# Kernel tuning notes

Measured on AMD Instinct MI355X. Metric: run time of the kernel, lower is better.

Reference implementation:

```python
import jax, jax.numpy as jnp
import numpy as np

N = 1048576
NUM_FREQS = 4
NUM_DIM = 3
NUM_QUANTS = 80
NUM_FEATS = 4
MIN_LOG2_FREQ = 1.0
MAX_LOG2_FREQ = 6.0
NUM_LINES = 2 * NUM_FREQS * NUM_DIM  # sin/cos x freq x axis = 24
LATENT = NUM_LINES * NUM_FEATS       # 96


def setup_inputs() -> dict:
    key = jax.random.key(0)
    ks = jax.random.split(key, 8)
    positions = jax.random.uniform(ks[0], (N, NUM_DIM), jnp.float32, -1.0, 1.0)
    d = jax.random.normal(ks[1], (N, NUM_DIM), jnp.float32)
    directions = d / jnp.linalg.norm(d, axis=-1, keepdims=True)
    grid = jax.random.normal(ks[2], (NUM_LINES, NUM_QUANTS, NUM_FEATS), jnp.float32) * 0.1
    w_geom1 = jax.random.normal(ks[3], (LATENT, 64), jnp.float32) * (1.0 / np.sqrt(LATENT))
    w_geom2 = jax.random.normal(ks[4], (64, 16), jnp.float32) * (1.0 / 8.0)
    w_color1 = jax.random.normal(ks[5], (31, 64), jnp.float32) * (1.0 / np.sqrt(31.0))
    w_color2 = jax.random.normal(ks[6], (64, 64), jnp.float32) * (1.0 / 8.0)
    w_color3 = jax.random.normal(ks[7], (64, 3), jnp.float32) * (1.0 / 8.0)
    return {"positions": positions, "directions": directions, "grid": grid,
            "w_geom1": w_geom1, "w_geom2": w_geom2,
            "w_color1": w_color1, "w_color2": w_color2, "w_color3": w_color3}


@jax.custom_vjp
def trunc_exp(x):
    return jnp.exp(x)

def _te_fwd(x):
    return jnp.exp(x), x

def _te_bwd(x, g):
    return (g * jnp.exp(jnp.clip(x, -15.0, 15.0)),)

trunc_exp.defvjp(_te_fwd, _te_bwd)


def spherical_harmonics16(d):
    # degree-4 (l=0..3) real SH basis, 16 components, torch-ngp coefficients
    x, y, z = d[:, 0], d[:, 1], d[:, 2]
    xx, yy, zz = x * x, y * y, z * z
    xy, yz, xz = x * y, y * z, x * z
    return jnp.stack([
        jnp.full_like(x, 0.28209479177387814),
        -0.48860251190291987 * y,
        0.48860251190291987 * z,
        -0.48860251190291987 * x,
        1.0925484305920792 * xy,
        -1.0925484305920792 * yz,
        0.94617469575755997 * zz - 0.31539156525251999,
        -1.0925484305920792 * xz,
        0.54627421529603959 * (xx - yy),
        -0.59004358992664352 * y * (3.0 * xx - yy),
        2.8906114426405538 * xy * z,
        -0.45704579946446572 * y * (4.0 * zz - xx - yy),
        0.37317633259011546 * z * (2.0 * zz - 3.0 * xx - 3.0 * yy),
        -0.45704579946446572 * x * (4.0 * zz - xx - yy),
        1.4453057213202769 * z * (xx - yy),
        -0.59004358992664352 * x * (xx - 3.0 * yy),
    ], axis=-1)  # [N, 16]


def qff1_encode(positions, grid):
    # frequencies 2^linspace(min,max,F)
    freqs = 2.0 ** jnp.linspace(MIN_LOG2_FREQ, MAX_LOG2_FREQ, NUM_FREQS).astype(jnp.float32)
    # phase: [N, D, F]
    p = positions[:, :, None] * freqs[None, None, :]
    coords = jnp.concatenate([jnp.sin(p), jnp.cos(p)], axis=-1)  # [N, D, 2F]
    coords = coords.transpose(0, 2, 1).reshape(positions.shape[0], NUM_LINES)  # [N, L]
    # map [-1,1] -> continuous grid coord and linearly interpolate 1D lines
    u = (coords + 1.0) * 0.5 * (NUM_QUANTS - 1)
    i0 = jnp.clip(jnp.floor(u).astype(jnp.int32), 0, NUM_QUANTS - 2)
    w = (u - i0.astype(u.dtype))[..., None]  # [N, L, 1]
    lidx = jnp.arange(NUM_LINES)[None, :]
    g0 = grid[lidx, i0]      # [N, L, C]
    g1 = grid[lidx, i0 + 1]  # [N, L, C]
    feat = g0 * (1.0 - w) + g1 * w
    return feat.reshape(positions.shape[0], LATENT)


def _forward(positions, directions, grid, w_geom1, w_geom2, w_color1, w_color2, w_color3):
    enc = qff1_encode(positions, grid)                    # [N, 96]
    h = jax.nn.relu(enc @ w_geom1)                        # [N, 64]
    f = h @ w_geom2                                       # [N, 16]
    raw_sigma, feature = f[:, :1], f[:, 1:]
    density = trunc_exp(raw_sigma - 1.0)                  # [N, 1]
    sh = spherical_harmonics16(directions)                # [N, 16]
    hc = jnp.concatenate([sh, feature], axis=-1)          # [N, 31]
    hc = jax.nn.relu(hc @ w_color1)
    hc = jax.nn.relu(hc @ w_color2)
    rgb = jax.nn.sigmoid(hc @ w_color3)                   # [N, 3]
    return rgb, density


def reference(positions, directions, grid, w_geom1, w_geom2, w_color1, w_color2, w_color3):
    return _forward(positions, directions, grid, w_geom1, w_geom2, w_color1, w_color2, w_color3)
```

## Files before the change

### kernel.cpp

```cpp
#include <hip/hip_runtime.h>
#include <stdint.h>


typedef _Float16 half8  __attribute__((ext_vector_type(8)));
typedef _Float16 h2     __attribute__((ext_vector_type(2)));
typedef float    f32x16 __attribute__((ext_vector_type(16)));

union FragU { uint32_t u[4]; uint4 q; half8 h; };
union H2U   { uint32_t u; h2 h; };

static __device__ __forceinline__ h2 bch2(uint32_t v) { H2U x; x.u = v; return x.h; }
static __device__ __forceinline__ uint32_t bcu(h2 v)  { H2U x; x.h = v; return x.u; }

static __device__ __forceinline__ h2 cvtpk(float lo, float hi) {
  return __builtin_bit_cast(h2, __builtin_amdgcn_cvt_pkrtz(lo, hi));
}
static __device__ __forceinline__ uint32_t pkrtz(float lo, float hi) {
  return bcu(cvtpk(lo, hi));
}
static __device__ __forceinline__ void plswap_u(uint32_t &a, uint32_t &b) {
  asm("v_permlane32_swap_b32 %0, %1" : "+v"(a), "+v"(b));
}
static __device__ __forceinline__ void plswap_f(float &a, float &b) {
  asm("v_permlane32_swap_b32 %0, %1" : "+v"(a), "+v"(b));
}
static __device__ __forceinline__ half8 mk_frag(uint32_t a, uint32_t b, uint32_t c, uint32_t d) {
  FragU f; f.u[0] = a; f.u[1] = b; f.u[2] = c; f.u[3] = d; return f.h;
}
static __device__ __forceinline__ uint32_t maxz(uint32_t v) {
  h2 h = bch2(v); h = __builtin_elementwise_max(h, (h2)(_Float16)0.0f); return bcu(h);
}
static __device__ __forceinline__ unsigned short f16b(float v) {
  _Float16 h = (_Float16)v; return __builtin_bit_cast(unsigned short, h);
}

#define MFMA(A, B, C) __builtin_amdgcn_mfma_f32_32x32x16_f16((A), (B), (C), 0, 0, 0)

#define W1OFF   0
#define W2OFF   13312
#define WC1OFF  17920
#define WC2OFF  23040
#define WC3OFF  32256
#define GROFF   36864
#define LDSZ    52224
#define WBYTES  36864

static __device__ __forceinline__ half8 ldwp(const unsigned char* s, int row, int off) {
  FragU f; f.q = *(const uint4*)(s + row + off);
  asm volatile("" : "+v"(f.u[0]), "+v"(f.u[1]), "+v"(f.u[2]), "+v"(f.u[3]));
  return f.h;
}

template<int BASE, bool RELU>
static __device__ __forceinline__ half8 packB(const f32x16& a) {
  uint32_t x = pkrtz(a[BASE + 0], a[BASE + 1]);
  uint32_t z = pkrtz(a[BASE + 2], a[BASE + 3]);
  uint32_t y = pkrtz(a[BASE + 4], a[BASE + 5]);
  uint32_t w = pkrtz(a[BASE + 6], a[BASE + 7]);
  if (RELU) { x = maxz(x); z = maxz(z); y = maxz(y); w = maxz(w); }
  plswap_u(x, y);
  plswap_u(z, w);
  return mk_frag(x, z, y, w);
}

template<int J>
static __device__ __forceinline__ void gather(const float* m, int gbase,
                                              float q0, float q1, float q2,
                                              const unsigned char* lds,
                                              uint32_t& w01, uint32_t& w23) {
  constexpr int jm = J % 6;
  constexpr int DIMP[6] = {0, 1, 1, 2, 2, 0};
  constexpr int LNS0[6] = {0, 1, 4, 5, 8, 9};
  constexpr int GOFFJ = (LNS0[jm] + (J < 6 ? 0 : 12)) * 640;
  float q = (DIMP[jm] == 0) ? q0 : ((DIMP[jm] == 1) ? q1 : q2);
  float r = fmaf(q, m[jm], (J < 6) ? 0.0f : 0.25f);
  r = __builtin_amdgcn_fractf(r);
  float s = __builtin_amdgcn_sinf(r);
  float u = fmaf(s, 39.5f, 39.5f);
  int i0 = (int)u;
  i0 = i0 < 0 ? 0 : (i0 > 78 ? 78 : i0);
  float w = u - (float)i0;
  const unsigned char* base = lds + gbase + GOFFJ + (i0 << 2);
  uint32_t a0 = *(const uint32_t*)(base);
  uint32_t b0 = *(const uint32_t*)(base + 4);
  uint32_t a1 = *(const uint32_t*)(base + 320);
  uint32_t b1 = *(const uint32_t*)(base + 324);
  h2 wh = cvtpk(w, w);
  h2 f01 = __builtin_elementwise_fma(bch2(b0) - bch2(a0), wh, bch2(a0));
  h2 f23 = __builtin_elementwise_fma(bch2(b1) - bch2(a1), wh, bch2(a1));
  w01 = bcu(f01);
  w23 = bcu(f23);
}

template<int T>
static __device__ __forceinline__ half8 enc2(const float* m, int gbase,
                                             float q0, float q1, float q2,
                                             const unsigned char* lds) {
  uint32_t a, b, c, d;
  gather<2 * T + 0>(m, gbase, q0, q1, q2, lds, a, b);
  gather<2 * T + 1>(m, gbase, q0, q1, q2, lds, c, d);
  return mk_frag(a, b, c, d);
}

__global__ __launch_bounds__(512, 2)
void qff_fwd(const float* __restrict__ pos, const float* __restrict__ dir,
             const float* __restrict__ grid,
             const float* __restrict__ w1, const float* __restrict__ w2,
             const float* __restrict__ wc1, const float* __restrict__ wc2,
             const float* __restrict__ wc3,
             float* __restrict__ out, int Npts) {
  __shared__ __align__(16) unsigned char smem[LDSZ];
  const int tid = threadIdx.x;

  for (int i = tid; i < WBYTES / 4; i += 512) ((uint32_t*)smem)[i] = 0;
  __syncthreads();
  for (int i = tid; i < 6144; i += 512)
    *(unsigned short*)(smem + W1OFF  + (i & 63) * 208 + (i >> 6) * 2) = f16b(w1[i]);
  for (int i = tid; i < 1024; i += 512)
    *(unsigned short*)(smem + W2OFF  + (i & 15) * 144 + (i >> 4) * 2) = f16b(w2[i]);
  for (int i = tid; i < 1984; i += 512)
    *(unsigned short*)(smem + WC1OFF + (i & 63) * 80  + (i >> 6) * 2) = f16b(wc1[i]);
  for (int i = tid; i < 4096; i += 512)
    *(unsigned short*)(smem + WC2OFF + (i & 63) * 144 + (i >> 6) * 2) = f16b(wc2[i]);
  for (int i = tid; i < 192; i += 512)
    *(unsigned short*)(smem + WC3OFF + (i % 3) * 144 + (i / 3) * 2) = f16b(wc3[i]);
  for (int i = tid; i < 1920; i += 512) {
    float4 v = ((const float4*)grid)[i];
    int line = i / 80, q = i - line * 80;
    uint32_t* dst = (uint32_t*)(smem + GROFF + line * 640 + q * 4);
    dst[0]  = (((uint32_t)f16b(v.y)) << 16) | f16b(v.x);
    dst[80] = (((uint32_t)f16b(v.w)) << 16) | f16b(v.z);
  }
  __syncthreads();

  const int lane = tid & 63;
  const int wid  = tid >> 6;
  const int g    = lane >> 5;
  const int o    = lane & 31;

  const int a13 = o * 208 + g * 16;
  const int a9  = o * 144 + g * 16;
  const int a5  = o * 80  + g * 16;
  half8 w1f[2][6], w2f[4], c1f[2][2], c2f[2][4], c3f[4];
#pragma unroll
  for (int t = 0; t < 6; ++t) {
    w1f[0][t] = ldwp(smem, a13, W1OFF + t * 32);
    w1f[1][t] = ldwp(smem, a13, W1OFF + 6656 + t * 32);
  }
#pragma unroll
  for (int t = 0; t < 4; ++t) {
    w2f[t]    = ldwp(smem, a9, W2OFF + t * 32);
    c2f[0][t] = ldwp(smem, a9, WC2OFF + t * 32);
    c2f[1][t] = ldwp(smem, a9, WC2OFF + 4608 + t * 32);
    c3f[t]    = ldwp(smem, a9, WC3OFF + t * 32);
  }
#pragma unroll
  for (int t = 0; t < 2; ++t) {
    c1f[0][t] = ldwp(smem, a5, WC1OFF + t * 32);
    c1f[1][t] = ldwp(smem, a5, WC1OFF + 2560 + t * 32);
  }

  constexpr float IV = 0.15915494309189535f;
  constexpr float F0 = 2.0f, F1 = 6.349604207872798f, F2 = 20.158736798317971f, F3 = 64.0f;
  const float M0c[6] = {F0*IV, F0*IV, F1*IV, F1*IV, F2*IV, F3*IV};
  const float M1c[6] = {F0*IV, F1*IV, F2*IV, F2*IV, F3*IV, F3*IV};
  float m[6];
#pragma unroll
  for (int j = 0; j < 6; ++j) m[j] = g ? M1c[j] : M0c[j];
  const int gbase = GROFF + g * 1280;

  const f32x16 Z = {0,0,0,0, 0,0,0,0, 0,0,0,0, 0,0,0,0};
  const int ntile = Npts >> 8;
  int tb = blockIdx.x;
  if (tb >= ntile) return;

  int p = (tb << 8) + (wid << 5) + o;
  float px = pos[3*p+0], py = pos[3*p+1], pz = pos[3*p+2];
  float dx = dir[3*p+0], dy = dir[3*p+1], dz = dir[3*p+2];

  for (; tb < ntile; tb += gridDim.x) {
    int tbn = tb + gridDim.x;
    int pn  = ((tbn < ntile ? tbn : ntile - 1) << 8) + (wid << 5) + o;
    float npx = pos[3*pn+0], npy = pos[3*pn+1], npz = pos[3*pn+2];
    float ndx = dir[3*pn+0], ndy = dir[3*pn+1], ndz = dir[3*pn+2];

    float q0 = g ? pz : px;
    float q1 = g ? px : py;
    float q2 = g ? py : pz;

    f32x16 acc0 = Z, acc1 = Z;
#define L1STEP(T) { half8 bf = enc2<T>(m, gbase, q0, q1, q2, smem); \
                    acc0 = MFMA(w1f[0][T], bf, acc0); \
                    acc1 = MFMA(w1f[1][T], bf, acc1); }
    L1STEP(0) L1STEP(1) L1STEP(2) L1STEP(3) L1STEP(4) L1STEP(5)
#undef L1STEP

    half8 hb0 = packB<0, true>(acc0), hb1 = packB<8, true>(acc0);
    half8 hb2 = packB<0, true>(acc1), hb3 = packB<8, true>(acc1);

    f32x16 acc2 = Z;
    acc2 = MFMA(w2f[0], hb0, acc2);
    acc2 = MFMA(w2f[1], hb1, acc2);
    acc2 = MFMA(w2f[2], hb2, acc2);
    acc2 = MFMA(w2f[3], hb3, acc2);
    float sigma = __expf(acc2[0] - 1.0f);

    float xx = dx*dx, yy = dy*dy, zz = dz*dz;
    float xy = dx*dy, yz = dy*dz, xz = dx*dz;
    float s0, s1, s2, s3, s4, s5, s6, s7;
    if (g == 0) {
      s0 = 0.28209479177387814f;
      s1 = -0.48860251190291987f * dy;
      s2 =  0.48860251190291987f * dz;
      s3 = -0.48860251190291987f * dx;
      s4 =  1.0925484305920792f * xy;
      s5 = -1.0925484305920792f * yz;
      s6 =  0.94617469575756f * zz - 0.31539156525252f;
      s7 = -1.0925484305920792f * xz;
    } else {
      s0 =  0.5462742152960396f * (xx - yy);
      s1 = -0.5900435899266435f * dy * (3.0f * xx - yy);
      s2 =  2.890611442640554f * xy * dz;
      s3 = -0.4570457994644657f * dy * (4.0f * zz - xx - yy);
      s4 =  0.37317633259011546f * dz * (2.0f * zz - 3.0f * xx - 3.0f * yy);
      s5 = -0.4570457994644657f * dx * (4.0f * zz - xx - yy);
      s6 =  1.445305721320277f * dz * (xx - yy);
      s7 = -0.5900435899266435f * dx * (xx - 3.0f * yy);
    }
    half8 shB = mk_frag(pkrtz(s0, s1), pkrtz(s2, s3), pkrtz(s4, s5), pkrtz(s6, s7));

    uint32_t e0 = pkrtz(acc2[1], acc2[2]);
    uint32_t e2 = pkrtz(acc2[5], acc2[6]);
    plswap_u(e0, e2);
    float a3 = acc2[3], b7 = acc2[7];
    plswap_f(a3, b7);
    float cc0 = acc2[0], d4 = acc2[4];
    plswap_f(cc0, d4);
    uint32_t e1 = pkrtz(a3, d4);
    uint32_t e3 = pkrtz(b7, acc2[4]);
    half8 featB = mk_frag(e0, e1, e2, e3);

    f32x16 acc3a = Z, acc3b = Z;
    acc3a = MFMA(c1f[0][0], shB,   acc3a);
    acc3a = MFMA(c1f[0][1], featB, acc3a);
    acc3b = MFMA(c1f[1][0], shB,   acc3b);
    acc3b = MFMA(c1f[1][1], featB, acc3b);

    half8 g2b0 = packB<0, true>(acc3a), g2b1 = packB<8, true>(acc3a);
    half8 g2b2 = packB<0, true>(acc3b), g2b3 = packB<8, true>(acc3b);

    f32x16 acc4a = Z, acc4b = Z;
    acc4a = MFMA(c2f[0][0], g2b0, acc4a);
    acc4a = MFMA(c2f[0][1], g2b1, acc4a);
    acc4a = MFMA(c2f[0][2], g2b2, acc4a);
    acc4a = MFMA(c2f[0][3], g2b3, acc4a);
    acc4b = MFMA(c2f[1][0], g2b0, acc4b);
    acc4b = MFMA(c2f[1][1], g2b1, acc4b);
    acc4b = MFMA(c2f[1][2], g2b2, acc4b);
    acc4b = MFMA(c2f[1][3], g2b3, acc4b);

    half8 g3b0 = packB<0, true>(acc4a), g3b1 = packB<8, true>(acc4a);
    half8 g3b2 = packB<0, true>(acc4b), g3b3 = packB<8, true>(acc4b);

    f32x16 acc5 = Z;
    acc5 = MFMA(c3f[0], g3b0, acc5);
    acc5 = MFMA(c3f[1], g3b1, acc5);
    acc5 = MFMA(c3f[2], g3b2, acc5);
    acc5 = MFMA(c3f[3], g3b3, acc5);

    if (lane < 32) {
      float rr = __builtin_amdgcn_rcpf(1.0f + __expf(-acc5[0]));
      float gg = __builtin_amdgcn_rcpf(1.0f + __expf(-acc5[1]));
      float bb = __builtin_amdgcn_rcpf(1.0f + __expf(-acc5[2]));
      out[3 * p + 0] = rr;
      out[3 * p + 1] = gg;
      out[3 * p + 2] = bb;
      out[3 * Npts + p] = sigma;
    }

    p = pn;
    px = npx; py = npy; pz = npz;
    dx = ndx; dy = ndy; dz = ndz;
  }
}

extern "C" void kernel_launch(void* const* d_in, const int* in_sizes, int n_in,
                              void* d_out, int out_size, void* d_ws, size_t ws_size,
                              hipStream_t stream) {
  const float* pos  = (const float*)d_in[0];
  const float* dirs = (const float*)d_in[1];
  const float* grid = (const float*)d_in[2];
  const float* w1   = (const float*)d_in[3];
  const float* w2   = (const float*)d_in[4];
  const float* wc1  = (const float*)d_in[5];
  const float* wc2  = (const float*)d_in[6];
  const float* wc3  = (const float*)d_in[7];
  float* out = (float*)d_out;
  const int Npts = in_sizes[0] / 3;

  qff_fwd<<<dim3(512), dim3(512), 0, stream>>>(pos, dirs, grid, w1, w2, wc1, wc2, wc3,
                                               out, Npts);
}
```

Baseline: 53.44 us.

## Reload MLP weight fragments from LDS per use to raise occupancy

Weight fragments are no longer held in registers for the whole kernel. Each MFMA now reloads its weight fragment from LDS, and the next-tile prefetch of positions and directions is dropped. This frees registers, so launch bounds go from 2 to 6 blocks per CU and the grid grows from 512 to 768 blocks. The cost is many more LDS reads per tile and no software prefetch of inputs, while LDS use (about 52 KB per block) may still cap the number of resident blocks.

```diff
diff --git a/kernel.cpp b/kernel.cpp
--- a/kernel.cpp
+++ b/kernel.cpp
@@ -45,10 +45,8 @@
 #define LDSZ    52224
 #define WBYTES  36864
 
-static __device__ __forceinline__ half8 ldwp(const unsigned char* s, int row, int off) {
-  FragU f; f.q = *(const uint4*)(s + row + off);
-  asm volatile("" : "+v"(f.u[0]), "+v"(f.u[1]), "+v"(f.u[2]), "+v"(f.u[3]));
-  return f.h;
+static __device__ __forceinline__ half8 ldw(const unsigned char* s, int row, int off) {
+  FragU f; f.q = *(const uint4*)(s + row + off); return f.h;
 }
 
 template<int BASE, bool RELU>
@@ -102,7 +100,7 @@
   return mk_frag(a, b, c, d);
 }
 
-__global__ __launch_bounds__(512, 2)
+__global__ __launch_bounds__(512, 6)
 void qff_fwd(const float* __restrict__ pos, const float* __restrict__ dir,
              const float* __restrict__ grid,
              const float* __restrict__ w1, const float* __restrict__ w2,
@@ -138,28 +136,6 @@
   const int g    = lane >> 5;
   const int o    = lane & 31;
 
-  const int a13 = o * 208 + g * 16;
-  const int a9  = o * 144 + g * 16;
-  const int a5  = o * 80  + g * 16;
-  half8 w1f[2][6], w2f[4], c1f[2][2], c2f[2][4], c3f[4];
-#pragma unroll
-  for (int t = 0; t < 6; ++t) {
-    w1f[0][t] = ldwp(smem, a13, W1OFF + t * 32);
-    w1f[1][t] = ldwp(smem, a13, W1OFF + 6656 + t * 32);
-  }
-#pragma unroll
-  for (int t = 0; t < 4; ++t) {
-    w2f[t]    = ldwp(smem, a9, W2OFF + t * 32);
-    c2f[0][t] = ldwp(smem, a9, WC2OFF + t * 32);
-    c2f[1][t] = ldwp(smem, a9, WC2OFF + 4608 + t * 32);
-    c3f[t]    = ldwp(smem, a9, WC3OFF + t * 32);
-  }
-#pragma unroll
-  for (int t = 0; t < 2; ++t) {
-    c1f[0][t] = ldwp(smem, a5, WC1OFF + t * 32);
-    c1f[1][t] = ldwp(smem, a5, WC1OFF + 2560 + t * 32);
-  }
-
   constexpr float IV = 0.15915494309189535f;
   constexpr float F0 = 2.0f, F1 = 6.349604207872798f, F2 = 20.158736798317971f, F3 = 64.0f;
   const float M0c[6] = {F0*IV, F0*IV, F1*IV, F1*IV, F2*IV, F3*IV};
@@ -168,21 +144,16 @@
 #pragma unroll
   for (int j = 0; j < 6; ++j) m[j] = g ? M1c[j] : M0c[j];
   const int gbase = GROFF + g * 1280;
+  const int a13 = o * 208 + g * 16;
+  const int a9  = o * 144 + g * 16;
+  const int a5  = o * 80  + g * 16;
 
   const f32x16 Z = {0,0,0,0, 0,0,0,0, 0,0,0,0, 0,0,0,0};
   const int ntile = Npts >> 8;
-  int tb = blockIdx.x;
-  if (tb >= ntile) return;
-
-  int p = (tb << 8) + (wid << 5) + o;
-  float px = pos[3*p+0], py = pos[3*p+1], pz = pos[3*p+2];
-  float dx = dir[3*p+0], dy = dir[3*p+1], dz = dir[3*p+2];
-
-  for (; tb < ntile; tb += gridDim.x) {
-    int tbn = tb + gridDim.x;
-    int pn  = ((tbn < ntile ? tbn : ntile - 1) << 8) + (wid << 5) + o;
-    float npx = pos[3*pn+0], npy = pos[3*pn+1], npz = pos[3*pn+2];
-    float ndx = dir[3*pn+0], ndy = dir[3*pn+1], ndz = dir[3*pn+2];
+
+  for (int tb = blockIdx.x; tb < ntile; tb += gridDim.x) {
+    const int p = (tb << 8) + (wid << 5) + o;
+    float px = pos[3*p+0], py = pos[3*p+1], pz = pos[3*p+2];
 
     float q0 = g ? pz : px;
     float q1 = g ? px : py;
@@ -190,8 +161,8 @@
 
     f32x16 acc0 = Z, acc1 = Z;
 #define L1STEP(T) { half8 bf = enc2<T>(m, gbase, q0, q1, q2, smem); \
-                    acc0 = MFMA(w1f[0][T], bf, acc0); \
-                    acc1 = MFMA(w1f[1][T], bf, acc1); }
+                    acc0 = MFMA(ldw(smem, a13, W1OFF + T*32), bf, acc0); \
+                    acc1 = MFMA(ldw(smem, a13, W1OFF + 6656 + T*32), bf, acc1); }
     L1STEP(0) L1STEP(1) L1STEP(2) L1STEP(3) L1STEP(4) L1STEP(5)
 #undef L1STEP
 
@@ -199,12 +170,13 @@
     half8 hb2 = packB<0, true>(acc1), hb3 = packB<8, true>(acc1);
 
     f32x16 acc2 = Z;
-    acc2 = MFMA(w2f[0], hb0, acc2);
-    acc2 = MFMA(w2f[1], hb1, acc2);
-    acc2 = MFMA(w2f[2], hb2, acc2);
-    acc2 = MFMA(w2f[3], hb3, acc2);
+    acc2 = MFMA(ldw(smem, a9, W2OFF +  0), hb0, acc2);
+    acc2 = MFMA(ldw(smem, a9, W2OFF + 32), hb1, acc2);
+    acc2 = MFMA(ldw(smem, a9, W2OFF + 64), hb2, acc2);
+    acc2 = MFMA(ldw(smem, a9, W2OFF + 96), hb3, acc2);
     float sigma = __expf(acc2[0] - 1.0f);
 
+    float dx = dir[3*p+0], dy = dir[3*p+1], dz = dir[3*p+2];
     float xx = dx*dx, yy = dy*dy, zz = dz*dz;
     float xy = dx*dy, yz = dy*dz, xz = dx*dz;
     float s0, s1, s2, s3, s4, s5, s6, s7;
@@ -241,32 +213,32 @@
     half8 featB = mk_frag(e0, e1, e2, e3);
 
     f32x16 acc3a = Z, acc3b = Z;
-    acc3a = MFMA(c1f[0][0], shB,   acc3a);
-    acc3a = MFMA(c1f[0][1], featB, acc3a);
-    acc3b = MFMA(c1f[1][0], shB,   acc3b);
-    acc3b = MFMA(c1f[1][1], featB, acc3b);
+    acc3a = MFMA(ldw(smem, a5, WC1OFF +  0), shB,   acc3a);
+    acc3a = MFMA(ldw(smem, a5, WC1OFF + 32), featB, acc3a);
+    acc3b = MFMA(ldw(smem, a5, WC1OFF + 2560 +  0), shB,   acc3b);
+    acc3b = MFMA(ldw(smem, a5, WC1OFF + 2560 + 32), featB, acc3b);
 
     half8 g2b0 = packB<0, true>(acc3a), g2b1 = packB<8, true>(acc3a);
     half8 g2b2 = packB<0, true>(acc3b), g2b3 = packB<8, true>(acc3b);
 
     f32x16 acc4a = Z, acc4b = Z;
-    acc4a = MFMA(c2f[0][0], g2b0, acc4a);
-    acc4a = MFMA(c2f[0][1], g2b1, acc4a);
-    acc4a = MFMA(c2f[0][2], g2b2, acc4a);
-    acc4a = MFMA(c2f[0][3], g2b3, acc4a);
-    acc4b = MFMA(c2f[1][0], g2b0, acc4b);
-    acc4b = MFMA(c2f[1][1], g2b1, acc4b);
-    acc4b = MFMA(c2f[1][2], g2b2, acc4b);
-    acc4b = MFMA(c2f[1][3], g2b3, acc4b);
+    acc4a = MFMA(ldw(smem, a9, WC2OFF +  0), g2b0, acc4a);
+    acc4a = MFMA(ldw(smem, a9, WC2OFF + 32), g2b1, acc4a);
+    acc4a = MFMA(ldw(smem, a9, WC2OFF + 64), g2b2, acc4a);
+    acc4a = MFMA(ldw(smem, a9, WC2OFF + 96), g2b3, acc4a);
+    acc4b = MFMA(ldw(smem, a9, WC2OFF + 4608 +  0), g2b0, acc4b);
+    acc4b = MFMA(ldw(smem, a9, WC2OFF + 4608 + 32), g2b1, acc4b);
+    acc4b = MFMA(ldw(smem, a9, WC2OFF + 4608 + 64), g2b2, acc4b);
+    acc4b = MFMA(ldw(smem, a9, WC2OFF + 4608 + 96), g2b3, acc4b);
 
     half8 g3b0 = packB<0, true>(acc4a), g3b1 = packB<8, true>(acc4a);
     half8 g3b2 = packB<0, true>(acc4b), g3b3 = packB<8, true>(acc4b);
 
     f32x16 acc5 = Z;
-    acc5 = MFMA(c3f[0], g3b0, acc5);
-    acc5 = MFMA(c3f[1], g3b1, acc5);
-    acc5 = MFMA(c3f[2], g3b2, acc5);
-    acc5 = MFMA(c3f[3], g3b3, acc5);
+    acc5 = MFMA(ldw(smem, a9, WC3OFF +  0), g3b0, acc5);
+    acc5 = MFMA(ldw(smem, a9, WC3OFF + 32), g3b1, acc5);
+    acc5 = MFMA(ldw(smem, a9, WC3OFF + 64), g3b2, acc5);
+    acc5 = MFMA(ldw(smem, a9, WC3OFF + 96), g3b3, acc5);
 
     if (lane < 32) {
       float rr = __builtin_amdgcn_rcpf(1.0f + __expf(-acc5[0]));
@@ -277,10 +249,6 @@
       out[3 * p + 2] = bb;
       out[3 * Npts + p] = sigma;
     }
-
-    p = pn;
-    px = npx; py = npy; pz = npz;
-    dx = ndx; dy = ndy; dz = ndz;
   }
 }
 
@@ -298,6 +266,6 @@
   float* out = (float*)d_out;
   const int Npts = in_sizes[0] / 3;
 
-  qff_fwd<<<dim3(512), dim3(512), 0, stream>>>(pos, dirs, grid, w1, w2, wc1, wc2, wc3,
+  qff_fwd<<<dim3(768), dim3(512), 0, stream>>>(pos, dirs, grid, w1, w2, wc1, wc2, wc3,
                                                out, Npts);
 }
```

New measurement: 75.87 us. +42.0%, slower.
